# Kernel optimization log

Hardware: AMD Instinct MI355X
Metric: run time of the kernel (lower is better)

The kernel has to match this reference:

```python
import jax, jax.numpy as jnp
import numpy as np

LN_EPS = 1e-5  # torch LayerNorm default

def _lnorm(x):
    # LayerNorm over last dim, no affine params
    mu = jnp.mean(x, axis=-1, keepdims=True)
    var = jnp.var(x, axis=-1, keepdims=True)
    return (x - mu) / jnp.sqrt(var + LN_EPS)

def setup_inputs() -> dict:
    key = jax.random.key(0)
    k0, k1, k2, k3 = jax.random.split(key, 4)
    B, S, D, H = 4, 4096, 1024, 64
    xs_q = jax.random.normal(k0, (B, S, D), dtype=jnp.float32)
    # torch Linear(D, H, bias=False) stores weight [H, D]; we store [D, H] = W.T
    sc = 1.0 / np.sqrt(D)
    Wq = jax.random.normal(k1, (D, H), dtype=jnp.float32) * sc
    Wk = jax.random.normal(k2, (D, H), dtype=jnp.float32) * sc
    Wv = jax.random.normal(k3, (D, H), dtype=jnp.float32) * sc
    return {"xs_q": xs_q, "Wq": Wq, "Wk": Wk, "Wv": Wv}

def reference(xs_q, Wq, Wk, Wv):
    # self-attention: xs_k_v = xs_q
    qs = _lnorm(jnp.einsum('bsd,dh->bsh', xs_q, Wq))  # [B,S,H]
    ks = _lnorm(jnp.einsum('bsd,dh->bsh', xs_q, Wk))
    vs = jnp.einsum('bsd,dh->bsh', xs_q, Wv)
    scaling = 1.0 / jnp.sqrt(jnp.asarray(qs.shape[-1], dtype=qs.dtype))
    att = jnp.einsum('bqh,bkh->bqk', qs, ks)          # [B,S,S] full attention matrix
    probs = jax.nn.softmax(scaling * att, axis=-1)
    vsp = jnp.einsum('bqk,bkh->bqh', probs, vs)       # [B,S,H]
    return vsp
```

## Files before the change

### kernel.cpp

```cpp
#include <hip/hip_runtime.h>
#include <hip/hip_bf16.h>


typedef __bf16 bf16x8 __attribute__((ext_vector_type(8)));
typedef __bf16 bf16x4 __attribute__((ext_vector_type(4)));
typedef float f32x4 __attribute__((ext_vector_type(4)));

#define NROW 16384
#define DD   1024
#define HH   64
#define SS   4096
#define LS   68

static __device__ inline unsigned short f2bf_u(float x) {
  __bf16 b = (__bf16)x;
  return __builtin_bit_cast(unsigned short, b);
}
static __device__ inline bf16x8 ld8(const __bf16* p) {
  bf16x4 lo = *reinterpret_cast<const bf16x4*>(p);
  bf16x4 hi = *reinterpret_cast<const bf16x4*>(p + 4);
  return __builtin_shufflevector(lo, hi, 0, 1, 2, 3, 4, 5, 6, 7);
}

__global__ __launch_bounds__(256) void k_transpose_w(
    const float* __restrict__ Wq, const float* __restrict__ Wk,
    const float* __restrict__ Wv, __bf16* __restrict__ WT) {
  int idx = blockIdx.x * 256 + threadIdx.x;
  int mat = idx >> 16;
  int rem = idx & 65535;
  int k = rem >> 6, h = rem & 63;
  const float* W = (mat == 0) ? Wq : ((mat == 1) ? Wk : Wv);
  WT[(size_t)(mat * 64 + h) * DD + k] = (__bf16)W[rem];
}

__global__ __launch_bounds__(128, 2) void k_proj(
    const float* __restrict__ X, const __bf16* __restrict__ WT,
    __bf16* __restrict__ qb, __bf16* __restrict__ kbp, __bf16* __restrict__ vT) {
  const int t = threadIdx.x, lane = t & 63, w = t >> 6;
  const int quad = lane >> 4, m = lane & 15;
  const int Mb = blockIdx.x * 32;
  const int row = Mb + 16 * w + m;
  const float* xp = &X[(size_t)row * DD + quad * 8];
  const __bf16* wp = &WT[(size_t)m * DD + quad * 8];

  f32x4 acc[12];
#pragma unroll
  for (int i = 0; i < 12; i++) acc[i] = (f32x4){0.f, 0.f, 0.f, 0.f};

  float4 xa = *reinterpret_cast<const float4*>(xp);
  float4 xb = *reinterpret_cast<const float4*>(xp + 4);
  bf16x8 wn[12];
#pragma unroll
  for (int nt = 0; nt < 12; nt++)
    wn[nt] = *reinterpret_cast<const bf16x8*>(wp + (size_t)nt * 16 * DD);

  for (int ko = 0; ko < DD; ko += 32) {
    bf16x8 a;
    a[0] = (__bf16)xa.x; a[1] = (__bf16)xa.y;
    a[2] = (__bf16)xa.z; a[3] = (__bf16)xa.w;
    a[4] = (__bf16)xb.x; a[5] = (__bf16)xb.y;
    a[6] = (__bf16)xb.z; a[7] = (__bf16)xb.w;
    bf16x8 wc[12];
#pragma unroll
    for (int nt = 0; nt < 12; nt++) wc[nt] = wn[nt];
    if (ko + 32 < DD) {
      xa = *reinterpret_cast<const float4*>(xp + ko + 32);
      xb = *reinterpret_cast<const float4*>(xp + ko + 36);
#pragma unroll
      for (int nt = 0; nt < 12; nt++)
        wn[nt] = *reinterpret_cast<const bf16x8*>(
            wp + (size_t)nt * 16 * DD + ko + 32);
    }
#pragma unroll
    for (int nt = 0; nt < 12; nt++)
      acc[nt] = __builtin_amdgcn_mfma_f32_16x16x32_bf16(a, wc[nt], acc[nt], 0, 0, 0);
  }

#pragma unroll
  for (int mat = 0; mat < 2; mat++) {
#pragma unroll
    for (int reg = 0; reg < 4; reg++) {
      float s = 0.f, s2 = 0.f;
#pragma unroll
      for (int ntl = 0; ntl < 4; ntl++) {
        float x = acc[mat * 4 + ntl][reg];
        s += x; s2 += x * x;
      }
#pragma unroll
      for (int off = 1; off < 16; off <<= 1) {
        s += __shfl_xor(s, off, 64);
        s2 += __shfl_xor(s2, off, 64);
      }
      float mu = s * (1.0f / 64.0f);
      float var = s2 * (1.0f / 64.0f) - mu * mu;
      float rstd = rsqrtf(var + 1e-5f);
      float scl = (mat == 0) ? 0.125f * 1.44269504f * rstd : rstd;
#pragma unroll
      for (int ntl = 0; ntl < 4; ntl++)
        acc[mat * 4 + ntl][reg] = (acc[mat * 4 + ntl][reg] - mu) * scl;
    }
  }

  const int rowbase = Mb + 16 * w + quad * 4;
#pragma unroll
  for (int nt = 0; nt < 4; nt++)
#pragma unroll
    for (int reg = 0; reg < 4; reg++) {
      qb[(size_t)(rowbase + reg) * HH + m + 16 * nt] = (__bf16)acc[nt][reg];
      kbp[(size_t)(rowbase + reg) * HH + m + 16 * nt] = (__bf16)acc[4 + nt][reg];
    }
  const int b = Mb >> 12;
  const int s0 = (Mb & 4095) + 16 * w + quad * 4;
#pragma unroll
  for (int nt = 0; nt < 4; nt++) {
    ushort4 pk = make_ushort4(f2bf_u(acc[8 + nt][0]), f2bf_u(acc[8 + nt][1]),
                              f2bf_u(acc[8 + nt][2]), f2bf_u(acc[8 + nt][3]));
    *reinterpret_cast<ushort4*>(
        &vT[((size_t)(b * 64) + m + 16 * nt) * SS + s0]) = pk;
  }
}

__global__ __launch_bounds__(256, 6) void k_attn(
    const __bf16* __restrict__ qb, const __bf16* __restrict__ kbp,
    const __bf16* __restrict__ vT, float* __restrict__ Op,
    float* __restrict__ lp, int spbits) {
  __shared__ __bf16 Klds[64 * LS];
  __shared__ __bf16 Vlds[64 * LS];
  __shared__ __bf16 Plds[4][16 * LS];
  const int t = threadIdx.x, lane = t & 63, w = t >> 6;
  const int quad = lane >> 4, m = lane & 15;
  const int nsp = 1 << spbits;
  const int qt = blockIdx.x >> spbits, sp = blockIdx.x & (nsp - 1);
  const int KPS = SS >> spbits;
  const int Mb = qt * 64;
  const int b = Mb >> 12;
  const size_t kvbase = (size_t)b * SS * HH;

  bf16x8 qf[2];
  {
    const int row = Mb + 16 * w + m;
    qf[0] = *reinterpret_cast<const bf16x8*>(&qb[(size_t)row * HH + quad * 8]);
    qf[1] = *reinterpret_cast<const bf16x8*>(&qb[(size_t)row * HH + 32 + quad * 8]);
  }
  bf16x8 ones;
#pragma unroll
  for (int i = 0; i < 8; i++) ones[i] = (__bf16)1.0f;

  f32x4 O[4], lac;
#pragma unroll
  for (int i = 0; i < 4; i++) O[i] = (f32x4){0.f, 0.f, 0.f, 0.f};
  lac = (f32x4){0.f, 0.f, 0.f, 0.f};

  const int c0row = t >> 3, ck0 = (t & 7) * 8;
  const int c1row = c0row + 32;
  const int kb_lo = sp * KPS, kb_hi = kb_lo + KPS;

  uint4 kd0, kd1, vd0, vd1;
  {
    kd0 = *reinterpret_cast<const uint4*>(&kbp[kvbase + (size_t)(kb_lo + c0row) * HH + ck0]);
    kd1 = *reinterpret_cast<const uint4*>(&kbp[kvbase + (size_t)(kb_lo + c1row) * HH + ck0]);
    vd0 = *reinterpret_cast<const uint4*>(&vT[(size_t)(b * 64 + c0row) * SS + kb_lo + ck0]);
    vd1 = *reinterpret_cast<const uint4*>(&vT[(size_t)(b * 64 + c1row) * SS + kb_lo + ck0]);
  }

  for (int kb0 = kb_lo; kb0 < kb_hi; kb0 += 64) {
    {
      __bf16* kp0 = &Klds[c0row * LS + ck0];
      __bf16* kp1 = &Klds[c1row * LS + ck0];
      __bf16* vp0 = &Vlds[c0row * LS + ck0];
      __bf16* vp1 = &Vlds[c1row * LS + ck0];
      *reinterpret_cast<uint2*>(kp0) = make_uint2(kd0.x, kd0.y);
      *reinterpret_cast<uint2*>(kp0 + 4) = make_uint2(kd0.z, kd0.w);
      *reinterpret_cast<uint2*>(kp1) = make_uint2(kd1.x, kd1.y);
      *reinterpret_cast<uint2*>(kp1 + 4) = make_uint2(kd1.z, kd1.w);
      *reinterpret_cast<uint2*>(vp0) = make_uint2(vd0.x, vd0.y);
      *reinterpret_cast<uint2*>(vp0 + 4) = make_uint2(vd0.z, vd0.w);
      *reinterpret_cast<uint2*>(vp1) = make_uint2(vd1.x, vd1.y);
      *reinterpret_cast<uint2*>(vp1 + 4) = make_uint2(vd1.z, vd1.w);
    }
    __syncthreads();
    if (kb0 + 64 < kb_hi) {
      kd0 = *reinterpret_cast<const uint4*>(&kbp[kvbase + (size_t)(kb0 + 64 + c0row) * HH + ck0]);
      kd1 = *reinterpret_cast<const uint4*>(&kbp[kvbase + (size_t)(kb0 + 64 + c1row) * HH + ck0]);
      vd0 = *reinterpret_cast<const uint4*>(&vT[(size_t)(b * 64 + c0row) * SS + kb0 + 64 + ck0]);
      vd1 = *reinterpret_cast<const uint4*>(&vT[(size_t)(b * 64 + c1row) * SS + kb0 + 64 + ck0]);
    }

    f32x4 sc[4];
#pragma unroll
    for (int nt = 0; nt < 4; nt++) sc[nt] = (f32x4){0.f, 0.f, 0.f, 0.f};
#pragma unroll
    for (int kk = 0; kk < 2; kk++)
#pragma unroll
      for (int nt = 0; nt < 4; nt++) {
        bf16x8 bf = ld8(&Klds[(m + 16 * nt) * LS + 32 * kk + quad * 8]);
        sc[nt] = __builtin_amdgcn_mfma_f32_16x16x32_bf16(qf[kk], bf, sc[nt], 0, 0, 0);
      }

    __bf16* Pw = Plds[w];
#pragma unroll
    for (int nt = 0; nt < 4; nt++)
#pragma unroll
      for (int reg = 0; reg < 4; reg++)
        Pw[(quad * 4 + reg) * LS + m + 16 * nt] = (__bf16)exp2f(sc[nt][reg]);

#pragma unroll
    for (int kk = 0; kk < 2; kk++) {
      bf16x8 pf = ld8(&Pw[m * LS + 32 * kk + quad * 8]);
      lac = __builtin_amdgcn_mfma_f32_16x16x32_bf16(ones, pf, lac, 0, 0, 0);
#pragma unroll
      for (int ht = 0; ht < 4; ht++) {
        bf16x8 vf = ld8(&Vlds[(m + 16 * ht) * LS + 32 * kk + quad * 8]);
        O[ht] = __builtin_amdgcn_mfma_f32_16x16x32_bf16(vf, pf, O[ht], 0, 0, 0);
      }
    }
    __syncthreads();
  }

  const int rowg = Mb + 16 * w + m;
  float4* obase = reinterpret_cast<float4*>(
      &Op[((size_t)sp * NROW + rowg) * HH + quad * 16]);
#pragma unroll
  for (int ht = 0; ht < 4; ht++)
    obase[ht] = make_float4(O[ht][0], O[ht][1], O[ht][2], O[ht][3]);
  if (quad == 0) lp[sp * NROW + rowg] = lac[0];
}

__global__ __launch_bounds__(256) void k_comb(const float* __restrict__ Op,
                                              const float* __restrict__ lp,
                                              float* __restrict__ out, int nsp) {
  int idx = blockIdx.x * 256 + threadIdx.x;
  int row = idx >> 6, h = idx & 63;
  int soff = ((h >> 2) & 3) * 16 + (h >> 4) * 4 + (h & 3);
  size_t sbase = (size_t)row * HH + soff;
  float o = 0.f, l = 0.f;
  for (int j = 0; j < nsp; j++) {
    o += Op[(size_t)j * NROW * HH + sbase];
    l += lp[j * NROW + row];
  }
  out[idx] = o / l;
}

extern "C" void kernel_launch(void* const* d_in, const int* in_sizes, int n_in,
                              void* d_out, int out_size, void* d_ws, size_t ws_size,
                              hipStream_t stream) {
  const float* X  = (const float*)d_in[0];
  const float* Wq = (const float*)d_in[1];
  const float* Wk = (const float*)d_in[2];
  const float* Wv = (const float*)d_in[3];
  float* out = (float*)d_out;
  char* ws = (char*)d_ws;

  __bf16* WT  = (__bf16*)(ws);
  __bf16* qb  = (__bf16*)(ws + (size_t)512 * 1024);
  __bf16* kbp = (__bf16*)(ws + (size_t)2560 * 1024);
  __bf16* vT  = (__bf16*)(ws + (size_t)4608 * 1024);
  float*  Op  = (float*)(ws + (size_t)6656 * 1024);
  const size_t need8 = (size_t)(6656 + 8 * 4096 + 512) * 1024;
  const int spbits = (ws_size >= need8) ? 3 : 2;
  const int nsp = 1 << spbits;
  float* lp = (float*)(ws + (size_t)(6656 + nsp * 4096) * 1024);

  hipLaunchKernelGGL(k_transpose_w, dim3(768), dim3(256), 0, stream, Wq, Wk, Wv, WT);
  hipLaunchKernelGGL(k_proj, dim3(NROW / 32), dim3(128), 0, stream, X, WT, qb, kbp, vT);
  hipLaunchKernelGGL(k_attn, dim3((NROW / 64) * nsp), dim3(256), 0, stream,
                     qb, kbp, vT, Op, lp, spbits);
  hipLaunchKernelGGL(k_comb, dim3(NROW * HH / 256), dim3(256), 0, stream,
                     Op, lp, out, nsp);
}
```

Baseline: 197.3 us.

## Split projection K dimension across four waves with LDS reduction

Result: no change. 195.4 us (-0.9%).

```diff
diff --git a/kernel.cpp b/kernel.cpp
--- a/kernel.cpp
+++ b/kernel.cpp
@@ -33,15 +33,16 @@
   WT[(size_t)(mat * 64 + h) * DD + k] = (__bf16)W[rem];
 }
 
-__global__ __launch_bounds__(128, 2) void k_proj(
+__global__ __launch_bounds__(256, 4) void k_proj(
     const float* __restrict__ X, const __bf16* __restrict__ WT,
     __bf16* __restrict__ qb, __bf16* __restrict__ kbp, __bf16* __restrict__ vT) {
+  __shared__ float red[2][64][52];
   const int t = threadIdx.x, lane = t & 63, w = t >> 6;
   const int quad = lane >> 4, m = lane & 15;
-  const int Mb = blockIdx.x * 32;
-  const int row = Mb + 16 * w + m;
-  const float* xp = &X[(size_t)row * DD + quad * 8];
-  const __bf16* wp = &WT[(size_t)m * DD + quad * 8];
+  const int Mb = blockIdx.x * 16;
+  const int k0 = w * 256 + quad * 8;
+  const float* xp = &X[(size_t)(Mb + m) * DD + k0];
+  const __bf16* wtp = &WT[(size_t)m * DD + k0];
 
   f32x4 acc[12];
 #pragma unroll
@@ -49,32 +50,52 @@
 
   float4 xa = *reinterpret_cast<const float4*>(xp);
   float4 xb = *reinterpret_cast<const float4*>(xp + 4);
-  bf16x8 wn[12];
+  bf16x8 bn[12];
 #pragma unroll
   for (int nt = 0; nt < 12; nt++)
-    wn[nt] = *reinterpret_cast<const bf16x8*>(wp + (size_t)nt * 16 * DD);
-
-  for (int ko = 0; ko < DD; ko += 32) {
+    bn[nt] = *reinterpret_cast<const bf16x8*>(wtp + (size_t)nt * 16 * DD);
+
+#pragma unroll
+  for (int it = 0; it < 8; it++) {
+    const int nxt = (it + 1) & 7;
     bf16x8 a;
     a[0] = (__bf16)xa.x; a[1] = (__bf16)xa.y;
     a[2] = (__bf16)xa.z; a[3] = (__bf16)xa.w;
     a[4] = (__bf16)xb.x; a[5] = (__bf16)xb.y;
     a[6] = (__bf16)xb.z; a[7] = (__bf16)xb.w;
-    bf16x8 wc[12];
-#pragma unroll
-    for (int nt = 0; nt < 12; nt++) wc[nt] = wn[nt];
-    if (ko + 32 < DD) {
-      xa = *reinterpret_cast<const float4*>(xp + ko + 32);
-      xb = *reinterpret_cast<const float4*>(xp + ko + 36);
-#pragma unroll
-      for (int nt = 0; nt < 12; nt++)
-        wn[nt] = *reinterpret_cast<const bf16x8*>(
-            wp + (size_t)nt * 16 * DD + ko + 32);
-    }
+    float4 nxa = *reinterpret_cast<const float4*>(xp + nxt * 32);
+    float4 nxb = *reinterpret_cast<const float4*>(xp + nxt * 32 + 4);
+#pragma unroll
+    for (int nt = 0; nt < 12; nt++) {
+      acc[nt] = __builtin_amdgcn_mfma_f32_16x16x32_bf16(a, bn[nt], acc[nt], 0, 0, 0);
+      bn[nt] = *reinterpret_cast<const bf16x8*>(
+          wtp + (size_t)nt * 16 * DD + nxt * 32);
+    }
+    xa = nxa; xb = nxb;
+  }
+
+  if (w >= 2) {
 #pragma unroll
     for (int nt = 0; nt < 12; nt++)
-      acc[nt] = __builtin_amdgcn_mfma_f32_16x16x32_bf16(a, wc[nt], acc[nt], 0, 0, 0);
-  }
+      *reinterpret_cast<f32x4*>(&red[w - 2][lane][nt * 4]) = acc[nt];
+  }
+  __syncthreads();
+  if (w < 2) {
+#pragma unroll
+    for (int nt = 0; nt < 12; nt++)
+      acc[nt] += *reinterpret_cast<const f32x4*>(&red[w][lane][nt * 4]);
+  }
+  __syncthreads();
+  if (w == 1) {
+#pragma unroll
+    for (int nt = 0; nt < 12; nt++)
+      *reinterpret_cast<f32x4*>(&red[0][lane][nt * 4]) = acc[nt];
+  }
+  __syncthreads();
+  if (w != 0) return;
+#pragma unroll
+  for (int nt = 0; nt < 12; nt++)
+    acc[nt] += *reinterpret_cast<const f32x4*>(&red[0][lane][nt * 4]);
 
 #pragma unroll
   for (int mat = 0; mat < 2; mat++) {
@@ -101,7 +122,7 @@
     }
   }
 
-  const int rowbase = Mb + 16 * w + quad * 4;
+  const int rowbase = Mb + quad * 4;
 #pragma unroll
   for (int nt = 0; nt < 4; nt++)
 #pragma unroll
@@ -110,7 +131,7 @@
       kbp[(size_t)(rowbase + reg) * HH + m + 16 * nt] = (__bf16)acc[4 + nt][reg];
     }
   const int b = Mb >> 12;
-  const int s0 = (Mb & 4095) + 16 * w + quad * 4;
+  const int s0 = (Mb & 4095) + quad * 4;
 #pragma unroll
   for (int nt = 0; nt < 4; nt++) {
     ushort4 pk = make_ushort4(f2bf_u(acc[8 + nt][0]), f2bf_u(acc[8 + nt][1]),
@@ -262,7 +283,7 @@
   float* lp = (float*)(ws + (size_t)(6656 + nsp * 4096) * 1024);
 
   hipLaunchKernelGGL(k_transpose_w, dim3(768), dim3(256), 0, stream, Wq, Wk, Wv, WT);
-  hipLaunchKernelGGL(k_proj, dim3(NROW / 32), dim3(128), 0, stream, X, WT, qb, kbp, vT);
+  hipLaunchKernelGGL(k_proj, dim3(NROW / 16), dim3(256), 0, stream, X, WT, qb, kbp, vT);
   hipLaunchKernelGGL(k_attn, dim3((NROW / 64) * nsp), dim3(256), 0, stream,
                      qb, kbp, vT, Op, lp, spbits);
   hipLaunchKernelGGL(k_comb, dim3(NROW * HH / 256), dim3(256), 0, stream,
```

## Stage X and W tiles through LDS with coalesced loads in projection kernel

Applied to the files above, without the earlier changes.

Result: faster. 164.1 us (-16.8%).

```diff
diff --git a/kernel.cpp b/kernel.cpp
--- a/kernel.cpp
+++ b/kernel.cpp
@@ -15,6 +15,10 @@
 static __device__ inline unsigned short f2bf_u(float x) {
   __bf16 b = (__bf16)x;
   return __builtin_bit_cast(unsigned short, b);
+}
+static __device__ inline uint2 pk4f(float a, float b, float c, float d) {
+  return make_uint2((unsigned)f2bf_u(a) | ((unsigned)f2bf_u(b) << 16),
+                    (unsigned)f2bf_u(c) | ((unsigned)f2bf_u(d) << 16));
 }
 static __device__ inline bf16x8 ld8(const __bf16* p) {
   bf16x4 lo = *reinterpret_cast<const bf16x4*>(p);
@@ -36,44 +40,70 @@
 __global__ __launch_bounds__(128, 2) void k_proj(
     const float* __restrict__ X, const __bf16* __restrict__ WT,
     __bf16* __restrict__ qb, __bf16* __restrict__ kbp, __bf16* __restrict__ vT) {
+  __shared__ __bf16 Xs[32 * LS];
+  __shared__ __bf16 Ws[192 * LS];
   const int t = threadIdx.x, lane = t & 63, w = t >> 6;
   const int quad = lane >> 4, m = lane & 15;
   const int Mb = blockIdx.x * 32;
-  const int row = Mb + 16 * w + m;
-  const float* xp = &X[(size_t)row * DD + quad * 8];
-  const __bf16* wp = &WT[(size_t)m * DD + quad * 8];
 
   f32x4 acc[12];
 #pragma unroll
   for (int i = 0; i < 12; i++) acc[i] = (f32x4){0.f, 0.f, 0.f, 0.f};
 
-  float4 xa = *reinterpret_cast<const float4*>(xp);
-  float4 xb = *reinterpret_cast<const float4*>(xp + 4);
-  bf16x8 wn[12];
-#pragma unroll
-  for (int nt = 0; nt < 12; nt++)
-    wn[nt] = *reinterpret_cast<const bf16x8*>(wp + (size_t)nt * 16 * DD);
-
-  for (int ko = 0; ko < DD; ko += 32) {
-    bf16x8 a;
-    a[0] = (__bf16)xa.x; a[1] = (__bf16)xa.y;
-    a[2] = (__bf16)xa.z; a[3] = (__bf16)xa.w;
-    a[4] = (__bf16)xb.x; a[5] = (__bf16)xb.y;
-    a[6] = (__bf16)xb.z; a[7] = (__bf16)xb.w;
-    bf16x8 wc[12];
-#pragma unroll
-    for (int nt = 0; nt < 12; nt++) wc[nt] = wn[nt];
-    if (ko + 32 < DD) {
-      xa = *reinterpret_cast<const float4*>(xp + ko + 32);
-      xb = *reinterpret_cast<const float4*>(xp + ko + 36);
-#pragma unroll
-      for (int nt = 0; nt < 12; nt++)
-        wn[nt] = *reinterpret_cast<const bf16x8*>(
-            wp + (size_t)nt * 16 * DD + ko + 32);
-    }
-#pragma unroll
-    for (int nt = 0; nt < 12; nt++)
-      acc[nt] = __builtin_amdgcn_mfma_f32_16x16x32_bf16(a, wc[nt], acc[nt], 0, 0, 0);
+  float4 xr[4];
+  bf16x8 wr[12];
+#pragma unroll
+  for (int i = 0; i < 4; i++) {
+    int c = t + i * 128, row = c >> 4, col = (c & 15) * 4;
+    xr[i] = *reinterpret_cast<const float4*>(&X[(size_t)(Mb + row) * DD + col]);
+  }
+#pragma unroll
+  for (int i = 0; i < 12; i++) {
+    int c = t + i * 128, row = c >> 3, col = (c & 7) * 8;
+    wr[i] = *reinterpret_cast<const bf16x8*>(&WT[(size_t)row * DD + col]);
+  }
+
+  for (int s = 0; s < 16; s++) {
+    if (s) __syncthreads();
+#pragma unroll
+    for (int i = 0; i < 4; i++) {
+      int c = t + i * 128, row = c >> 4, col = (c & 15) * 4;
+      *reinterpret_cast<uint2*>(&Xs[row * LS + col]) =
+          pk4f(xr[i].x, xr[i].y, xr[i].z, xr[i].w);
+    }
+#pragma unroll
+    for (int i = 0; i < 12; i++) {
+      int c = t + i * 128, row = c >> 3, col = (c & 7) * 8;
+      uint4 raw = __builtin_bit_cast(uint4, wr[i]);
+      __bf16* wd = &Ws[row * LS + col];
+      *reinterpret_cast<uint2*>(wd) = make_uint2(raw.x, raw.y);
+      *reinterpret_cast<uint2*>(wd + 4) = make_uint2(raw.z, raw.w);
+    }
+    __syncthreads();
+    if (s + 1 < 16) {
+      const int ko = (s + 1) * 64;
+#pragma unroll
+      for (int i = 0; i < 4; i++) {
+        int c = t + i * 128, row = c >> 4, col = (c & 15) * 4;
+        xr[i] = *reinterpret_cast<const float4*>(
+            &X[(size_t)(Mb + row) * DD + ko + col]);
+      }
+#pragma unroll
+      for (int i = 0; i < 12; i++) {
+        int c = t + i * 128, row = c >> 3, col = (c & 7) * 8;
+        wr[i] = *reinterpret_cast<const bf16x8*>(
+            &WT[(size_t)row * DD + ko + col]);
+      }
+    }
+#pragma unroll
+    for (int kk = 0; kk < 2; kk++) {
+      bf16x8 a = ld8(&Xs[(16 * w + m) * LS + 32 * kk + quad * 8]);
+#pragma unroll
+      for (int nt = 0; nt < 12; nt++) {
+        bf16x8 bfr = ld8(&Ws[(16 * nt + m) * LS + 32 * kk + quad * 8]);
+        acc[nt] = __builtin_amdgcn_mfma_f32_16x16x32_bf16(a, bfr, acc[nt], 0, 0, 0);
+      }
+    }
   }
 
 #pragma unroll
```
